# Optimization experiments

Hardware: AMD Instinct MI355X
Metric: run time of the kernel (lower is better)

## Reference

```python
import jax, jax.numpy as jnp
import numpy as np

N_MI, N_DI = 100000, 50000   # node counts
E, L = 500000, 200000        # message edges, supervision (label) edges
F_MI, F_DI, H = 256, 128, 128


def setup_inputs() -> dict:
    key = jax.random.key(0)
    ks = iter(jax.random.split(key, 40))

    def nrm(shape, scale):
        return jax.random.normal(next(ks), shape, jnp.float32) * scale

    inp = {
        'x_mi': jax.random.normal(next(ks), (N_MI, F_MI), jnp.float32),
        'x_di': jax.random.normal(next(ks), (N_DI, F_DI), jnp.float32),
        'W_mi': nrm((H, F_MI), 1.0 / np.sqrt(F_MI)),
        'b_mi': jnp.zeros((H,), jnp.float32),
        'W_di': nrm((H, F_DI), 1.0 / np.sqrt(F_DI)),
        'b_di': jnp.zeros((H,), jnp.float32),
        'emb_mi': nrm((N_MI, H), 1.0),
        'emb_di': nrm((N_DI, H), 1.0),
    }
    # SAGEConv weights per layer per relation (md: miRNA->disease, dm: reverse)
    dims = [(H, 256), (256, 128), (128, 64)]
    for i, (ci, co) in enumerate(dims, 1):
        for rel in ('md', 'dm'):
            inp[f'Wl{i}_{rel}'] = nrm((co, ci), 1.0 / np.sqrt(ci))  # neighbor lin (with bias)
            inp[f'bl{i}_{rel}'] = jnp.zeros((co,), jnp.float32)
            inp[f'Wr{i}_{rel}'] = nrm((co, ci), 1.0 / np.sqrt(ci))  # root lin (no bias)
    inp['edge_src'] = jax.random.randint(next(ks), (E,), 0, N_MI)
    inp['edge_dst'] = jax.random.randint(next(ks), (E,), 0, N_DI)
    inp['label_src'] = jax.random.randint(next(ks), (L,), 0, N_MI)
    inp['label_dst'] = jax.random.randint(next(ks), (L,), 0, N_DI)
    return inp


def _sage(x_src, x_dst, src, dst, n_dst, Wl, bl, Wr):
    # PyG SAGEConv (mean aggr): out = lin_l(mean_neighbors) + lin_r(x_dst)
    agg = jax.ops.segment_sum(x_src[src], dst, num_segments=n_dst)
    deg = jax.ops.segment_sum(jnp.ones_like(dst, dtype=x_src.dtype), dst, num_segments=n_dst)
    mean = agg / jnp.maximum(deg, 1.0)[:, None]
    return mean @ Wl.T + bl + x_dst @ Wr.T


def reference(x_mi, x_di, W_mi, b_mi, W_di, b_di, emb_mi, emb_di,
              Wl1_md, bl1_md, Wr1_md, Wl1_dm, bl1_dm, Wr1_dm,
              Wl2_md, bl2_md, Wr2_md, Wl2_dm, bl2_dm, Wr2_dm,
              Wl3_md, bl3_md, Wr3_md, Wl3_dm, bl3_dm, Wr3_dm,
              edge_src, edge_dst, label_src, label_dst):
    # node_id == arange(num_nodes), so the embedding lookup is the full table
    h_mi = x_mi @ W_mi.T + b_mi + emb_mi
    h_di = x_di @ W_di.T + b_di + emb_di
    layers = [((Wl1_md, bl1_md, Wr1_md), (Wl1_dm, bl1_dm, Wr1_dm)),
              ((Wl2_md, bl2_md, Wr2_md), (Wl2_dm, bl2_dm, Wr2_dm)),
              ((Wl3_md, bl3_md, Wr3_md), (Wl3_dm, bl3_dm, Wr3_dm))]
    for li, (pmd, pdm) in enumerate(layers):
        new_di = _sage(h_mi, h_di, edge_src, edge_dst, N_DI, *pmd)  # miRNA -> disease
        new_mi = _sage(h_di, h_mi, edge_dst, edge_src, N_MI, *pdm)  # disease -> miRNA (reverse)
        if li < 2:
            new_mi, new_di = jax.nn.relu(new_mi), jax.nn.relu(new_di)
        h_mi, h_di = new_mi, new_di
    # classifier: dot product on supervision edges -> [L]
    return (h_mi[label_src] * h_di[label_dst]).sum(axis=-1)
```

## Files before the change

### kernel.cpp

```cpp
#include <hip/hip_runtime.h>

#define N_MI 100000
#define N_DI 50000
#define MI_P 100352
#define DI_P 50176

#define SCAN_CHUNK 2048
#define NB_DI ((N_DI + SCAN_CHUNK - 1) / SCAN_CHUNK)
#define NB_MI ((N_MI + SCAN_CHUNK - 1) / SCAN_CHUNK)

typedef _Float16 half8  __attribute__((ext_vector_type(8)));
typedef _Float16 half4  __attribute__((ext_vector_type(4)));
typedef float    floatx4 __attribute__((ext_vector_type(4)));

__global__ void count_kernel(const int* __restrict__ src, const int* __restrict__ dst,
                             int* deg_mi, int* deg_di, int E) {
    int i = blockIdx.x * blockDim.x + threadIdx.x;
    if (i < E) {
        atomicAdd(&deg_mi[src[i]], 1);
        atomicAdd(&deg_di[dst[i]], 1);
    }
}

__global__ __launch_bounds__(256) void scan_part_kernel(const int* __restrict__ deg_di,
                                                        const int* __restrict__ deg_mi,
                                                        int* __restrict__ row_di,
                                                        int* __restrict__ row_mi,
                                                        int* __restrict__ bsum) {
    const int* deg; int* row; int n; int* bs;
    if (blockIdx.y == 0) { deg = deg_di; row = row_di; n = N_DI; bs = bsum; }
    else                 { deg = deg_mi; row = row_mi; n = N_MI; bs = bsum + 64; }
    int nb = (n + SCAN_CHUNK - 1) / SCAN_CHUNK;
    if ((int)blockIdx.x >= nb) return;
    int t = threadIdx.x;
    int base = blockIdx.x * SCAN_CHUNK + t * 8;
    int v[8]; int s = 0;
    #pragma unroll
    for (int e = 0; e < 8; ++e) {
        int i = base + e;
        v[e] = (i < n) ? deg[i] : 0;
        s += v[e];
    }
    int lane = t & 63, w = t >> 6;
    int x = s;
    #pragma unroll
    for (int off = 1; off < 64; off <<= 1) {
        int y = __shfl_up(x, off, 64);
        if (lane >= off) x += y;
    }
    __shared__ int wsum[4];
    if (lane == 63) wsum[w] = x;
    __syncthreads();
    int woff = 0;
    #pragma unroll
    for (int i = 0; i < 3; ++i) if (i < w) woff += wsum[i];
    int run = woff + x - s;
    #pragma unroll
    for (int e = 0; e < 8; ++e) {
        int i = base + e;
        if (i < n) row[i] = run;
        run += v[e];
    }
    if (t == 255) bs[blockIdx.x] = woff + x;
}

__global__ void scan_sums_kernel(int* __restrict__ bsum, int* __restrict__ row_di,
                                 int* __restrict__ row_mi) {
    int w = threadIdx.x >> 6, lane = threadIdx.x & 63;
    int nb = (w == 0) ? NB_DI : NB_MI;
    int* bs = bsum + w * 64;
    int v = (lane < nb) ? bs[lane] : 0;
    int x = v;
    #pragma unroll
    for (int off = 1; off < 64; off <<= 1) {
        int y = __shfl_up(x, off, 64);
        if (lane >= off) x += y;
    }
    if (lane < nb) bs[lane] = x - v;
    if (lane == nb - 1) {
        if (w == 0) row_di[N_DI] = x;
        else        row_mi[N_MI] = x;
    }
}

__global__ __launch_bounds__(256) void scan_add_kernel(const int* __restrict__ bsum,
                                                       int* __restrict__ row_di,
                                                       int* __restrict__ row_mi) {
    int* row; int n; const int* bs;
    if (blockIdx.y == 0) { row = row_di; n = N_DI; bs = bsum; }
    else                 { row = row_mi; n = N_MI; bs = bsum + 64; }
    int nb = (n + SCAN_CHUNK - 1) / SCAN_CHUNK;
    int b = blockIdx.x;
    if (b >= nb || b == 0) return;
    int off = bs[b];
    int base = b * SCAN_CHUNK + threadIdx.x;
    #pragma unroll
    for (int e = 0; e < 8; ++e) {
        int i = base + e * 256;
        if (i < n) row[i] += off;
    }
}

__global__ void fill_kernel(const int* __restrict__ src, const int* __restrict__ dst,
                            const int* __restrict__ row_mi, const int* __restrict__ row_di,
                            int* cur_mi, int* cur_di, int* csr_mi, int* csr_di, int E) {
    int i = blockIdx.x * blockDim.x + threadIdx.x;
    if (i >= E) return;
    int s = src[i], d = dst[i];
    int p = atomicAdd(&cur_di[d], 1);
    csr_di[row_di[d] + p] = s;
    int q = atomicAdd(&cur_mi[s], 1);
    csr_mi[row_mi[s] + q] = d;
}


struct CvtW {
    const float* s[14];
    _Float16* d[14];
    int K[14];
    int KI[14];
    int nch[14];
};

__global__ void cvtw_kernel(CvtW a) {
    int arr = blockIdx.y;
    int c = blockIdx.x * blockDim.x + threadIdx.x;
    if (c >= a.nch[arr]) return;
    int K = a.K[arr], KI = a.KI[arr];
    int lane = c & 63;
    int j = (c >> 6) & 3;
    int rest = c >> 8;
    int k = rest % KI;
    int p = rest / KI;
    int row = p * 64 + j * 16 + (lane & 15);
    int kcol = k * 32 + (lane >> 4) * 8;
    const float* s = a.s[arr] + (long)row * K + kcol;
    float4 u = *(const float4*)s;
    float4 v = *(const float4*)(s + 4);
    half8 h = {(_Float16)u.x, (_Float16)u.y, (_Float16)u.z, (_Float16)u.w,
               (_Float16)v.x, (_Float16)v.y, (_Float16)v.z, (_Float16)v.w};
    *(half8*)(a.d[arr] + (long)c * 8) = h;
}

template<int K>
__global__ __launch_bounds__(256) void cvt_frag(const float* __restrict__ in,
                                                _Float16* __restrict__ out, int M) {
    constexpr int KI = K / 32;
    constexpr int CPR = K / 8;
    __shared__ _Float16 lds[64 * (K + 8)];
    const int tile = blockIdx.x;
    const int tid = threadIdx.x;
    #pragma unroll
    for (int it = 0; it < KI; ++it) {
        int c = tid + it * 256;
        int r = c / CPR, col = c % CPR;
        int row = tile * 64 + r;
        if (row >= M) row = M - 1;
        const float* g = in + (long)row * K + col * 8;
        float4 u = *(const float4*)g;
        float4 v = *(const float4*)(g + 4);
        half8 h = {(_Float16)u.x, (_Float16)u.y, (_Float16)u.z, (_Float16)u.w,
                   (_Float16)v.x, (_Float16)v.y, (_Float16)v.z, (_Float16)v.w};
        *(half8*)&lds[r * (K + 8) + col * 8] = h;
    }
    __syncthreads();
    #pragma unroll
    for (int it = 0; it < KI; ++it) {
        int c = tid + it * 256;
        int lane = c & 63, i = (c >> 6) & 3, k = c >> 8;
        half8 h = *(const half8*)&lds[(i * 16 + (lane & 15)) * (K + 8) + k * 32 + (lane >> 4) * 8];
        *(half8*)(out + ((long)tile * 8 * K + c) * 8) = h;
    }
}

template<int DIN>
__global__ __launch_bounds__(256) void agg2_kernel(const _Float16* __restrict__ hsrc,
                                                   const int* __restrict__ row,
                                                   const int* __restrict__ csr,
                                                   _Float16* __restrict__ outf, int n) {
    constexpr int LPR = DIN / 8;
    constexpr int GR  = 64 / LPR;
    constexpr int KI  = DIN / 32;
    int node = blockIdx.x * 4 + (threadIdx.x >> 6);
    if (node >= n) return;
    int lane = threadIdx.x & 63;
    int g = lane / LPR, c = lane % LPR;
    int beg = row[node], end = row[node + 1];
    float acc[8] = {};
    #pragma unroll 2
    for (int j = beg + g; j < end; j += GR) {
        half8 v = *(const half8*)(hsrc + (long)csr[j] * DIN + c * 8);
        #pragma unroll
        for (int e = 0; e < 8; ++e) acc[e] += (float)v[e];
    }
    float inv = 1.f / (float)max(end - beg, 1);
    half8 o;
    #pragma unroll
    for (int e = 0; e < 8; ++e) {
        float s = acc[e];
        s += __shfl_down(s, 32);
        if (GR == 4) s += __shfl_down(s, 16);
        o[e] = (_Float16)(s * inv);
    }
    if (g == 0) {
        int mt = node >> 6, ii = (node >> 4) & 3, lrm = node & 15;
        long off = (((long)mt * KI + (c >> 2)) * 4 + ii) * 512 + (lrm + 16 * (c & 3)) * 8;
        *(half8*)(outf + off) = o;
    }
}

template<int KI, bool DUAL, int MR>
__global__ __launch_bounds__(256, 4) void hgemm_f(
    const _Float16* __restrict__ A1f, const _Float16* __restrict__ W1f,
    const _Float16* __restrict__ A2f, const _Float16* __restrict__ W2f,
    const float* __restrict__ bias, const float* __restrict__ Cadd,
    _Float16* __restrict__ C, _Float16* __restrict__ Cf, int M, int N, int relu)
{
    const int wave = threadIdx.x >> 6, lane = threadIdx.x & 63;
    const int quad = lane >> 4, lr = lane & 15;
    const int g0 = (blockIdx.x * 4 + wave) * MR;
    const int mt = g0 >> 2, i0 = g0 & 3;
    const int p = blockIdx.y;
    const long abase = ((long)(mt * KI * 4 + i0)) * 512 + lane * 8;
    const long wbase = ((long)p * KI * 4) * 512 + lane * 8;

    __shared__ _Float16 lds[4][MR * 16 * 72];
    _Float16* lw = lds[wave];

    floatx4 acc[MR][4] = {};

    #pragma unroll
    for (int pass = 0; pass < (DUAL ? 2 : 1); ++pass) {
        const _Float16* A = pass ? A2f : A1f;
        const _Float16* W = pass ? W2f : W1f;
        #pragma unroll
        for (int k = 0; k < KI; ++k) {
            half8 af[MR], bf[4];
            #pragma unroll
            for (int i = 0; i < MR; ++i)
                af[i] = *(const half8*)(A + abase + (k * 4 + i) * 512);
            #pragma unroll
            for (int j = 0; j < 4; ++j)
                bf[j] = *(const half8*)(W + wbase + (k * 4 + j) * 512);
            #pragma unroll
            for (int i = 0; i < MR; ++i)
                #pragma unroll
                for (int j = 0; j < 4; ++j)
                    acc[i][j] = __builtin_amdgcn_mfma_f32_16x16x32_f16(af[i], bf[j], acc[i][j], 0, 0, 0);
        }
    }

    const int m0 = g0 * 16, n0 = p * 64;
    #pragma unroll
    for (int ii = 0; ii < MR; ++ii) {
        #pragma unroll
        for (int j = 0; j < 4; ++j) {
            int n = n0 + j * 16 + lr;
            float bn = bias[n];
            #pragma unroll
            for (int r = 0; r < 4; ++r) {
                int m = m0 + ii * 16 + quad * 4 + r;
                float v = acc[ii][j][r] + bn;
                if (Cadd && m < M) v += Cadd[(long)m * N + n];
                if (relu) v = fmaxf(v, 0.f);
                lw[(ii * 16 + quad * 4 + r) * 72 + j * 16 + lr] = (_Float16)v;
            }
        }
    }
    __syncthreads();

    const int r2 = lane >> 3, cs = lane & 7;
    #pragma unroll
    for (int ii = 0; ii < MR * 2; ++ii) {
        int m = m0 + ii * 8 + r2;
        if (m < M)
            *(half8*)(C + (long)m * N + n0 + cs * 8) =
                *(const half8*)&lw[(ii * 8 + r2) * 72 + cs * 8];
    }

    if (Cf) {
        const int KIn = N >> 5;
        #pragma unroll
        for (int ii = 0; ii < MR; ++ii) {
            #pragma unroll
            for (int k2 = 0; k2 < 2; ++k2) {
                half8 h = *(const half8*)&lw[(ii * 16 + lr) * 72 + k2 * 32 + quad * 8];
                *(half8*)(Cf + ((long)(mt * KIn + p * 2 + k2) * 4 + i0 + ii) * 512 + lane * 8) = h;
            }
        }
    }
}

__global__ void classify_kernel(const _Float16* __restrict__ hmi, const _Float16* __restrict__ hdi,
                                const int* __restrict__ ls, const int* __restrict__ ld,
                                float* __restrict__ out, int L) {
    long idx = (long)blockIdx.x * blockDim.x + threadIdx.x;
    int e = (int)(idx >> 4), q = (int)(idx & 15);
    if (e >= L) return;
    const half4* ra = (const half4*)(hmi + (long)ls[e] * 64);
    const half4* rb = (const half4*)(hdi + (long)ld[e] * 64);
    half4 a = ra[q], b = rb[q];
    float s = (float)a.x * (float)b.x + (float)a.y * (float)b.y +
              (float)a.z * (float)b.z + (float)a.w * (float)b.w;
    #pragma unroll
    for (int off = 8; off >= 1; off >>= 1) s += __shfl_down(s, off, 16);
    if (q == 0) out[e] = s;
}

extern "C" void kernel_launch(void* const* d_in, const int* in_sizes, int n_in,
                              void* d_out, int out_size, void* d_ws, size_t ws_size,
                              hipStream_t stream) {
    const float* x_mi   = (const float*)d_in[0];
    const float* x_di   = (const float*)d_in[1];
    const float* W_mi   = (const float*)d_in[2];
    const float* b_mi   = (const float*)d_in[3];
    const float* W_di   = (const float*)d_in[4];
    const float* b_di   = (const float*)d_in[5];
    const float* emb_mi = (const float*)d_in[6];
    const float* emb_di = (const float*)d_in[7];
    const float* Wl1_md = (const float*)d_in[8];
    const float* bl1_md = (const float*)d_in[9];
    const float* Wr1_md = (const float*)d_in[10];
    const float* Wl1_dm = (const float*)d_in[11];
    const float* bl1_dm = (const float*)d_in[12];
    const float* Wr1_dm = (const float*)d_in[13];
    const float* Wl2_md = (const float*)d_in[14];
    const float* bl2_md = (const float*)d_in[15];
    const float* Wr2_md = (const float*)d_in[16];
    const float* Wl2_dm = (const float*)d_in[17];
    const float* bl2_dm = (const float*)d_in[18];
    const float* Wr2_dm = (const float*)d_in[19];
    const float* Wl3_md = (const float*)d_in[20];
    const float* bl3_md = (const float*)d_in[21];
    const float* Wr3_md = (const float*)d_in[22];
    const float* Wl3_dm = (const float*)d_in[23];
    const float* bl3_dm = (const float*)d_in[24];
    const float* Wr3_dm = (const float*)d_in[25];
    const int* edge_src  = (const int*)d_in[26];
    const int* edge_dst  = (const int*)d_in[27];
    const int* label_src = (const int*)d_in[28];
    const int* label_dst = (const int*)d_in[29];
    const int E = in_sizes[26];
    const int L = in_sizes[28];
    float* out = (float*)d_out;

    _Float16* hp = (_Float16*)d_ws;
    _Float16* wWmi  = hp; hp += 128 * 256;
    _Float16* wWdi  = hp; hp += 128 * 128;
    _Float16* wl1md = hp; hp += 256 * 128;
    _Float16* wr1md = hp; hp += 256 * 128;
    _Float16* wl1dm = hp; hp += 256 * 128;
    _Float16* wr1dm = hp; hp += 256 * 128;
    _Float16* wl2md = hp; hp += 128 * 256;
    _Float16* wr2md = hp; hp += 128 * 256;
    _Float16* wl2dm = hp; hp += 128 * 256;
    _Float16* wr2dm = hp; hp += 128 * 256;
    _Float16* wl3md = hp; hp += 64 * 128;
    _Float16* wr3md = hp; hp += 64 * 128;
    _Float16* wl3dm = hp; hp += 64 * 128;
    _Float16* wr3dm = hp; hp += 64 * 128;
    _Float16* h_mi0 = hp; hp += (long)MI_P * 128;
    _Float16* h_mi1 = hp; hp += (long)MI_P * 256;
    _Float16* h_di0 = hp; hp += (long)DI_P * 128;
    _Float16* h_di1 = hp; hp += (long)DI_P * 256;
    _Float16* hfa_mi = hp; hp += (long)MI_P * 128;
    _Float16* hfb_mi = hp; hp += (long)MI_P * 256;
    _Float16* hfa_di = hp; hp += (long)DI_P * 128;
    _Float16* hfb_di = hp; hp += (long)DI_P * 256;
    _Float16* agghf  = hp; hp += (long)MI_P * 256;

    int* ip = (int*)hp;
    int* deg_di = ip;  ip += N_DI;
    int* deg_mi = ip;  ip += N_MI;
    int* cur_di = ip;  ip += N_DI;
    int* cur_mi = ip;  ip += N_MI;
    int* row_di = ip;  ip += N_DI + 1;
    int* row_mi = ip;  ip += N_MI + 1;
    int* csr_di = ip;  ip += E;
    int* csr_mi = ip;  ip += E;
    int* bsum   = ip;  ip += 128;

    hipMemsetAsync(deg_di, 0, (size_t)(2 * (N_DI + N_MI)) * sizeof(int), stream);
    int eb = (E + 255) / 256;
    count_kernel<<<eb, 256, 0, stream>>>(edge_src, edge_dst, deg_mi, deg_di, E);
    scan_part_kernel<<<dim3(NB_MI, 2), 256, 0, stream>>>(deg_di, deg_mi, row_di, row_mi, bsum);
    scan_sums_kernel<<<1, 128, 0, stream>>>(bsum, row_di, row_mi);
    scan_add_kernel<<<dim3(NB_MI, 2), 256, 0, stream>>>(bsum, row_di, row_mi);
    fill_kernel<<<eb, 256, 0, stream>>>(edge_src, edge_dst, row_mi, row_di,
                                        cur_mi, cur_di, csr_mi, csr_di, E);

    CvtW cw;
    const float* srcs[14] = {W_mi, W_di, Wl1_md, Wr1_md, Wl1_dm, Wr1_dm,
                             Wl2_md, Wr2_md, Wl2_dm, Wr2_dm, Wl3_md, Wr3_md, Wl3_dm, Wr3_dm};
    _Float16* dsts[14] = {wWmi, wWdi, wl1md, wr1md, wl1dm, wr1dm,
                          wl2md, wr2md, wl2dm, wr2dm, wl3md, wr3md, wl3dm, wr3dm};
    int Ks[14]  = {256, 128, 128, 128, 128, 128, 256, 256, 256, 256, 128, 128, 128, 128};
    int Ns[14]  = {128, 128, 256, 256, 256, 256, 128, 128, 128, 128, 64, 64, 64, 64};
    for (int i = 0; i < 14; ++i) {
        cw.s[i] = srcs[i]; cw.d[i] = dsts[i];
        cw.K[i] = Ks[i]; cw.KI[i] = Ks[i] / 32;
        cw.nch[i] = Ns[i] * Ks[i] / 8;
    }
    cvtw_kernel<<<dim3(16, 14), 256, 0, stream>>>(cw);

    cvt_frag<256><<<MI_P / 64, 256, 0, stream>>>(x_mi, hfb_mi, N_MI);
    cvt_frag<128><<<DI_P / 64, 256, 0, stream>>>(x_di, hfb_di, N_DI);

    hgemm_f<8, false, 2><<<dim3(MI_P / 128, 2), 256, 0, stream>>>(
        hfb_mi, wWmi, nullptr, nullptr, b_mi, emb_mi, h_mi0, hfa_mi, N_MI, 128, 0);
    hgemm_f<4, false, 1><<<dim3(DI_P / 64, 2), 256, 0, stream>>>(
        hfb_di, wWdi, nullptr, nullptr, b_di, emb_di, h_di0, hfa_di, N_DI, 128, 0);

    agg2_kernel<128><<<(N_DI + 3) / 4, 256, 0, stream>>>(h_mi0, row_di, csr_di, agghf, N_DI);
    hgemm_f<4, true, 1><<<dim3(DI_P / 64, 4), 256, 0, stream>>>(
        agghf, wl1md, hfa_di, wr1md, bl1_md, nullptr, h_di1, hfb_di, N_DI, 256, 1);
    agg2_kernel<128><<<(N_MI + 3) / 4, 256, 0, stream>>>(h_di0, row_mi, csr_mi, agghf, N_MI);
    hgemm_f<4, true, 2><<<dim3(MI_P / 128, 4), 256, 0, stream>>>(
        agghf, wl1dm, hfa_mi, wr1dm, bl1_dm, nullptr, h_mi1, hfb_mi, N_MI, 256, 1);

    agg2_kernel<256><<<(N_DI + 3) / 4, 256, 0, stream>>>(h_mi1, row_di, csr_di, agghf, N_DI);
    hgemm_f<8, true, 1><<<dim3(DI_P / 64, 2), 256, 0, stream>>>(
        agghf, wl2md, hfb_di, wr2md, bl2_md, nullptr, h_di0, hfa_di, N_DI, 128, 1);
    agg2_kernel<256><<<(N_MI + 3) / 4, 256, 0, stream>>>(h_di1, row_mi, csr_mi, agghf, N_MI);
    hgemm_f<8, true, 2><<<dim3(MI_P / 128, 2), 256, 0, stream>>>(
        agghf, wl2dm, hfb_mi, wr2dm, bl2_dm, nullptr, h_mi0, hfa_mi, N_MI, 128, 1);

    agg2_kernel<128><<<(N_DI + 3) / 4, 256, 0, stream>>>(h_mi0, row_di, csr_di, agghf, N_DI);
    hgemm_f<4, true, 1><<<dim3(DI_P / 64, 1), 256, 0, stream>>>(
        agghf, wl3md, hfa_di, wr3md, bl3_md, nullptr, h_di1, nullptr, N_DI, 64, 0);
    agg2_kernel<128><<<(N_MI + 3) / 4, 256, 0, stream>>>(
        h_di0, row_mi, csr_mi, agghf, N_MI);
    hgemm_f<4, true, 1><<<dim3(MI_P / 64, 1), 256, 0, stream>>>(
        agghf, wl3dm, hfa_mi, wr3dm, bl3_dm, nullptr, h_mi1, nullptr, N_MI, 64, 0);

    classify_kernel<<<((long)L * 16 + 255) / 256, 256, 0, stream>>>(
        h_mi1, h_di1, label_src, label_dst, out, L);
}
```

Measured before the change: 827.2 us.

## Merge independent preprocessing launches into combined heterogeneous kernels

Degree counting, weight conversion and input fragment conversion now run as one launch, partitioned by block index. CSR fill and the two input-projection GEMMs run as a second combined launch. Separately, the embedding add in the input GEMM epilogue now uses vectorised row-wise float4 loads instead of scalar strided reads. The aim is to cut kernel launch and serialization gaps and let independent work overlap. The cost is that the merged kernels reserve the largest shared-memory footprint for every block, and that atomic-heavy blocks share the GPU with GEMM blocks.

```diff
diff --git a/kernel.cpp b/kernel.cpp
--- a/kernel.cpp
+++ b/kernel.cpp
@@ -12,15 +12,6 @@
 typedef _Float16 half8  __attribute__((ext_vector_type(8)));
 typedef _Float16 half4  __attribute__((ext_vector_type(4)));
 typedef float    floatx4 __attribute__((ext_vector_type(4)));
-
-__global__ void count_kernel(const int* __restrict__ src, const int* __restrict__ dst,
-                             int* deg_mi, int* deg_di, int E) {
-    int i = blockIdx.x * blockDim.x + threadIdx.x;
-    if (i < E) {
-        atomicAdd(&deg_mi[src[i]], 1);
-        atomicAdd(&deg_di[dst[i]], 1);
-    }
-}
 
 __global__ __launch_bounds__(256) void scan_part_kernel(const int* __restrict__ deg_di,
                                                         const int* __restrict__ deg_mi,
@@ -101,18 +92,6 @@
     }
 }
 
-__global__ void fill_kernel(const int* __restrict__ src, const int* __restrict__ dst,
-                            const int* __restrict__ row_mi, const int* __restrict__ row_di,
-                            int* cur_mi, int* cur_di, int* csr_mi, int* csr_di, int E) {
-    int i = blockIdx.x * blockDim.x + threadIdx.x;
-    if (i >= E) return;
-    int s = src[i], d = dst[i];
-    int p = atomicAdd(&cur_di[d], 1);
-    csr_di[row_di[d] + p] = s;
-    int q = atomicAdd(&cur_mi[s], 1);
-    csr_mi[row_mi[s] + q] = d;
-}
-
 
 struct CvtW {
     const float* s[14];
@@ -122,9 +101,9 @@
     int nch[14];
 };
 
-__global__ void cvtw_kernel(CvtW a) {
-    int arr = blockIdx.y;
-    int c = blockIdx.x * blockDim.x + threadIdx.x;
+__device__ __forceinline__ void cvtw_body(const CvtW& a, int b) {
+    int arr = b / 16;
+    int c = (b % 16) * 256 + threadIdx.x;
     if (c >= a.nch[arr]) return;
     int K = a.K[arr], KI = a.KI[arr];
     int lane = c & 63;
@@ -143,12 +122,11 @@
 }
 
 template<int K>
-__global__ __launch_bounds__(256) void cvt_frag(const float* __restrict__ in,
-                                                _Float16* __restrict__ out, int M) {
+__device__ __forceinline__ void cvt_frag_body(const float* __restrict__ in,
+                                              _Float16* __restrict__ out, int M,
+                                              int tile, _Float16* lds) {
     constexpr int KI = K / 32;
     constexpr int CPR = K / 8;
-    __shared__ _Float16 lds[64 * (K + 8)];
-    const int tile = blockIdx.x;
     const int tid = threadIdx.x;
     #pragma unroll
     for (int it = 0; it < KI; ++it) {
@@ -171,6 +149,34 @@
         half8 h = *(const half8*)&lds[(i * 16 + (lane & 15)) * (K + 8) + k * 32 + (lane >> 4) * 8];
         *(half8*)(out + ((long)tile * 8 * K + c) * 8) = h;
     }
+}
+
+struct Prep {
+    const int* src; const int* dst;
+    int* deg_mi; int* deg_di;
+    int E; int ncount;
+    CvtW cw;
+    const float* xmi; const float* xdi;
+    _Float16* ofmi; _Float16* ofdi;
+};
+
+__global__ __launch_bounds__(256) void prep_kernel(Prep a) {
+    __shared__ _Float16 lds[64 * 264];
+    int b = blockIdx.x;
+    if (b < a.ncount) {
+        int i = b * 256 + threadIdx.x;
+        if (i < a.E) {
+            atomicAdd(&a.deg_mi[a.src[i]], 1);
+            atomicAdd(&a.deg_di[a.dst[i]], 1);
+        }
+        return;
+    }
+    b -= a.ncount;
+    if (b < 224) { cvtw_body(a.cw, b); return; }
+    b -= 224;
+    if (b < MI_P / 64) { cvt_frag_body<256>(a.xmi, a.ofmi, N_MI, b, lds); return; }
+    b -= MI_P / 64;
+    cvt_frag_body<128>(a.xdi, a.ofdi, N_DI, b, lds);
 }
 
 template<int DIN>
@@ -209,23 +215,21 @@
     }
 }
 
-template<int KI, bool DUAL, int MR>
-__global__ __launch_bounds__(256, 4) void hgemm_f(
+template<int KI, bool DUAL, int MR, bool CADD>
+__device__ __forceinline__ void hgemm_body(
     const _Float16* __restrict__ A1f, const _Float16* __restrict__ W1f,
     const _Float16* __restrict__ A2f, const _Float16* __restrict__ W2f,
     const float* __restrict__ bias, const float* __restrict__ Cadd,
-    _Float16* __restrict__ C, _Float16* __restrict__ Cf, int M, int N, int relu)
+    _Float16* __restrict__ C, _Float16* __restrict__ Cf,
+    int M, int N, int relu, int bx, int p, _Float16* lds)
 {
     const int wave = threadIdx.x >> 6, lane = threadIdx.x & 63;
     const int quad = lane >> 4, lr = lane & 15;
-    const int g0 = (blockIdx.x * 4 + wave) * MR;
+    const int g0 = (bx * 4 + wave) * MR;
     const int mt = g0 >> 2, i0 = g0 & 3;
-    const int p = blockIdx.y;
     const long abase = ((long)(mt * KI * 4 + i0)) * 512 + lane * 8;
     const long wbase = ((long)p * KI * 4) * 512 + lane * 8;
-
-    __shared__ _Float16 lds[4][MR * 16 * 72];
-    _Float16* lw = lds[wave];
+    _Float16* lw = lds + wave * (MR * 16 * 72);
 
     floatx4 acc[MR][4] = {};
 
@@ -255,14 +259,11 @@
     for (int ii = 0; ii < MR; ++ii) {
         #pragma unroll
         for (int j = 0; j < 4; ++j) {
-            int n = n0 + j * 16 + lr;
-            float bn = bias[n];
+            float bn = bias[n0 + j * 16 + lr];
             #pragma unroll
             for (int r = 0; r < 4; ++r) {
-                int m = m0 + ii * 16 + quad * 4 + r;
                 float v = acc[ii][j][r] + bn;
-                if (Cadd && m < M) v += Cadd[(long)m * N + n];
-                if (relu) v = fmaxf(v, 0.f);
+                if (!CADD && relu) v = fmaxf(v, 0.f);
                 lw[(ii * 16 + quad * 4 + r) * 72 + j * 16 + lr] = (_Float16)v;
             }
         }
@@ -273,10 +274,26 @@
     #pragma unroll
     for (int ii = 0; ii < MR * 2; ++ii) {
         int m = m0 + ii * 8 + r2;
+        half8 h = *(const half8*)&lw[(ii * 8 + r2) * 72 + cs * 8];
+        if (CADD) {
+            if (m < M) {
+                const float* g = Cadd + (long)m * N + n0 + cs * 8;
+                float4 u = *(const float4*)g;
+                float4 v = *(const float4*)(g + 4);
+                float t[8] = {u.x, u.y, u.z, u.w, v.x, v.y, v.z, v.w};
+                #pragma unroll
+                for (int e = 0; e < 8; ++e) {
+                    float x = (float)h[e] + t[e];
+                    if (relu) x = fmaxf(x, 0.f);
+                    h[e] = (_Float16)x;
+                }
+            }
+            *(half8*)&lw[(ii * 8 + r2) * 72 + cs * 8] = h;
+        }
         if (m < M)
-            *(half8*)(C + (long)m * N + n0 + cs * 8) =
-                *(const half8*)&lw[(ii * 8 + r2) * 72 + cs * 8];
-    }
+            *(half8*)(C + (long)m * N + n0 + cs * 8) = h;
+    }
+    if (CADD) __syncthreads();
 
     if (Cf) {
         const int KIn = N >> 5;
@@ -289,6 +306,54 @@
             }
         }
     }
+}
+
+template<int KI, bool DUAL, int MR>
+__global__ __launch_bounds__(256, 4) void hgemm_f(
+    const _Float16* __restrict__ A1f, const _Float16* __restrict__ W1f,
+    const _Float16* __restrict__ A2f, const _Float16* __restrict__ W2f,
+    const float* __restrict__ bias,
+    _Float16* __restrict__ C, _Float16* __restrict__ Cf, int M, int N, int relu)
+{
+    __shared__ _Float16 lds[4 * MR * 16 * 72];
+    hgemm_body<KI, DUAL, MR, false>(A1f, W1f, A2f, W2f, bias, nullptr,
+                                    C, Cf, M, N, relu, blockIdx.x, blockIdx.y, lds);
+}
+
+struct FusedInit {
+    const int* src; const int* dst;
+    const int* row_mi; const int* row_di;
+    int* cur_mi; int* cur_di; int* csr_mi; int* csr_di;
+    int E; int nfill;
+    const _Float16* Ami; const _Float16* Wmi; const float* bmi; const float* embmi;
+    _Float16* Cmi; _Float16* Cfmi;
+    const _Float16* Adi; const _Float16* Wdi; const float* bdi; const float* embdi;
+    _Float16* Cdi; _Float16* Cfdi;
+};
+
+__global__ __launch_bounds__(256, 4) void fused_init_kernel(FusedInit a) {
+    __shared__ _Float16 lds[4 * 2 * 16 * 72];
+    int b = blockIdx.x;
+    if (b < a.nfill) {
+        int i = b * 256 + threadIdx.x;
+        if (i < a.E) {
+            int s = a.src[i], d = a.dst[i];
+            int p = atomicAdd(&a.cur_di[d], 1);
+            a.csr_di[a.row_di[d] + p] = s;
+            int q = atomicAdd(&a.cur_mi[s], 1);
+            a.csr_mi[a.row_mi[s] + q] = d;
+        }
+        return;
+    }
+    b -= a.nfill;
+    if (b < (MI_P / 128) * 2) {
+        hgemm_body<8, false, 2, true>(a.Ami, a.Wmi, nullptr, nullptr, a.bmi, a.embmi,
+                                      a.Cmi, a.Cfmi, N_MI, 128, 0, b >> 1, b & 1, lds);
+        return;
+    }
+    b -= (MI_P / 128) * 2;
+    hgemm_body<4, false, 1, true>(a.Adi, a.Wdi, nullptr, nullptr, a.bdi, a.embdi,
+                                  a.Cdi, a.Cfdi, N_DI, 128, 0, b >> 1, b & 1, lds);
 }
 
 __global__ void classify_kernel(const _Float16* __restrict__ hmi, const _Float16* __restrict__ hdi,
@@ -380,16 +445,14 @@
     int* csr_mi = ip;  ip += E;
     int* bsum   = ip;  ip += 128;
 
+    int eb = (E + 255) / 256;
+
     hipMemsetAsync(deg_di, 0, (size_t)(2 * (N_DI + N_MI)) * sizeof(int), stream);
-    int eb = (E + 255) / 256;
-    count_kernel<<<eb, 256, 0, stream>>>(edge_src, edge_dst, deg_mi, deg_di, E);
-    scan_part_kernel<<<dim3(NB_MI, 2), 256, 0, stream>>>(deg_di, deg_mi, row_di, row_mi, bsum);
-    scan_sums_kernel<<<1, 128, 0, stream>>>(bsum, row_di, row_mi);
-    scan_add_kernel<<<dim3(NB_MI, 2), 256, 0, stream>>>(bsum, row_di, row_mi);
-    fill_kernel<<<eb, 256, 0, stream>>>(edge_src, edge_dst, row_mi, row_di,
-                                        cur_mi, cur_di, csr_mi, csr_di, E);
-
-    CvtW cw;
+
+    Prep pr;
+    pr.src = edge_src; pr.dst = edge_dst;
+    pr.deg_mi = deg_mi; pr.deg_di = deg_di;
+    pr.E = E; pr.ncount = eb;
     const float* srcs[14] = {W_mi, W_di, Wl1_md, Wr1_md, Wl1_dm, Wr1_dm,
                              Wl2_md, Wr2_md, Wl2_dm, Wr2_dm, Wl3_md, Wr3_md, Wl3_dm, Wr3_dm};
     _Float16* dsts[14] = {wWmi, wWdi, wl1md, wr1md, wl1dm, wr1dm,
@@ -397,41 +460,51 @@
     int Ks[14]  = {256, 128, 128, 128, 128, 128, 256, 256, 256, 256, 128, 128, 128, 128};
     int Ns[14]  = {128, 128, 256, 256, 256, 256, 128, 128, 128, 128, 64, 64, 64, 64};
     for (int i = 0; i < 14; ++i) {
-        cw.s[i] = srcs[i]; cw.d[i] = dsts[i];
-        cw.K[i] = Ks[i]; cw.KI[i] = Ks[i] / 32;
-        cw.nch[i] = Ns[i] * Ks[i] / 8;
-    }
-    cvtw_kernel<<<dim3(16, 14), 256, 0, stream>>>(cw);
-
-    cvt_frag<256><<<MI_P / 64, 256, 0, stream>>>(x_mi, hfb_mi, N_MI);
-    cvt_frag<128><<<DI_P / 64, 256, 0, stream>>>(x_di, hfb_di, N_DI);
-
-    hgemm_f<8, false, 2><<<dim3(MI_P / 128, 2), 256, 0, stream>>>(
-        hfb_mi, wWmi, nullptr, nullptr, b_mi, emb_mi, h_mi0, hfa_mi, N_MI, 128, 0);
-    hgemm_f<4, false, 1><<<dim3(DI_P / 64, 2), 256, 0, stream>>>(
-        hfb_di, wWdi, nullptr, nullptr, b_di, emb_di, h_di0, hfa_di, N_DI, 128, 0);
+        pr.cw.s[i] = srcs[i]; pr.cw.d[i] = dsts[i];
+        pr.cw.K[i] = Ks[i]; pr.cw.KI[i] = Ks[i] / 32;
+        pr.cw.nch[i] = Ns[i] * Ks[i] / 8;
+    }
+    pr.xmi = x_mi; pr.xdi = x_di; pr.ofmi = hfb_mi; pr.ofdi = hfb_di;
+    int prep_blocks = eb + 224 + MI_P / 64 + DI_P / 64;
+    prep_kernel<<<prep_blocks, 256, 0, stream>>>(pr);
+
+    scan_part_kernel<<<dim3(NB_MI, 2), 256, 0, stream>>>(deg_di, deg_mi, row_di, row_mi, bsum);
+    scan_sums_kernel<<<1, 128, 0, stream>>>(bsum, row_di, row_mi);
+    scan_add_kernel<<<dim3(NB_MI, 2), 256, 0, stream>>>(bsum, row_di, row_mi);
+
+    FusedInit fi;
+    fi.src = edge_src; fi.dst = edge_dst;
+    fi.row_mi = row_mi; fi.row_di = row_di;
+    fi.cur_mi = cur_mi; fi.cur_di = cur_di;
+    fi.csr_mi = csr_mi; fi.csr_di = csr_di;
+    fi.E = E; fi.nfill = eb;
+    fi.Ami = hfb_mi; fi.Wmi = wWmi; fi.bmi = b_mi; fi.embmi = emb_mi;
+    fi.Cmi = h_mi0; fi.Cfmi = hfa_mi;
+    fi.Adi = hfb_di; fi.Wdi = wWdi; fi.bdi = b_di; fi.embdi = emb_di;
+    fi.Cdi = h_di0; fi.Cfdi = hfa_di;
+    int fused_blocks = eb + (MI_P / 128) * 2 + (DI_P / 64) * 2;
+    fused_init_kernel<<<fused_blocks, 256, 0, stream>>>(fi);
 
     agg2_kernel<128><<<(N_DI + 3) / 4, 256, 0, stream>>>(h_mi0, row_di, csr_di, agghf, N_DI);
     hgemm_f<4, true, 1><<<dim3(DI_P / 64, 4), 256, 0, stream>>>(
-        agghf, wl1md, hfa_di, wr1md, bl1_md, nullptr, h_di1, hfb_di, N_DI, 256, 1);
+        agghf, wl1md, hfa_di, wr1md, bl1_md, h_di1, hfb_di, N_DI, 256, 1);
     agg2_kernel<128><<<(N_MI + 3) / 4, 256, 0, stream>>>(h_di0, row_mi, csr_mi, agghf, N_MI);
     hgemm_f<4, true, 2><<<dim3(MI_P / 128, 4), 256, 0, stream>>>(
-        agghf, wl1dm, hfa_mi, wr1dm, bl1_dm, nullptr, h_mi1, hfb_mi, N_MI, 256, 1);
+        agghf, wl1dm, hfa_mi, wr1dm, bl1_dm, h_mi1, hfb_mi, N_MI, 256, 1);
 
     agg2_kernel<256><<<(N_DI + 3) / 4, 256, 0, stream>>>(h_mi1, row_di, csr_di, agghf, N_DI);
     hgemm_f<8, true, 1><<<dim3(DI_P / 64, 2), 256, 0, stream>>>(
-        agghf, wl2md, hfb_di, wr2md, bl2_md, nullptr, h_di0, hfa_di, N_DI, 128, 1);
+        agghf, wl2md, hfb_di, wr2md, bl2_md, h_di0, hfa_di, N_DI, 128, 1);
     agg2_kernel<256><<<(N_MI + 3) / 4, 256, 0, stream>>>(h_di1, row_mi, csr_mi, agghf, N_MI);
     hgemm_f<8, true, 2><<<dim3(MI_P / 128, 2), 256, 0, stream>>>(
-        agghf, wl2dm, hfb_mi, wr2dm, bl2_dm, nullptr, h_mi0, hfa_mi, N_MI, 128, 1);
+        agghf, wl2dm, hfb_mi, wr2dm, bl2_dm, h_mi0, hfa_mi, N_MI, 128, 1);
 
     agg2_kernel<128><<<(N_DI + 3) / 4, 256, 0, stream>>>(h_mi0, row_di, csr_di, agghf, N_DI);
     hgemm_f<4, true, 1><<<dim3(DI_P / 64, 1), 256, 0, stream>>>(
-        agghf, wl3md, hfa_di, wr3md, bl3_md, nullptr, h_di1, nullptr, N_DI, 64, 0);
-    agg2_kernel<128><<<(N_MI + 3) / 4, 256, 0, stream>>>(
-        h_di0, row_mi, csr_mi, agghf, N_MI);
+        agghf, wl3md, hfa_di, wr3md, bl3_md, h_di1, nullptr, N_DI, 64, 0);
+    agg2_kernel<128><<<(N_MI + 3) / 4, 256, 0, stream>>>(h_di0, row_mi, csr_mi, agghf, N_MI);
     hgemm_f<4, true, 1><<<dim3(MI_P / 64, 1), 256, 0, stream>>>(
-        agghf, wl3dm, hfa_mi, wr3dm, bl3_dm, nullptr, h_mi1, nullptr, N_MI, 64, 0);
+        agghf, wl3dm, hfa_mi, wr3dm, bl3_dm, h_mi1, nullptr, N_MI, 64, 0);
 
     classify_kernel<<<((long)L * 16 + 255) / 256, 256, 0, stream>>>(
         h_mi1, h_di1, label_src, label_dst, out, L);
```

After: 776.7 us. 1.07x faster.
